# Kernel optimization log

Measured on AMD Instinct MI355X. Metric: run time of the kernel, lower is better.

The kernel has to match this reference:

```python
import jax, jax.numpy as jnp
import numpy as np

B, T, C = 4, 2048, 1024
N_HEAD = 16
HEAD = C // N_HEAD  # 64


def _rope_tables(T, dim, base=10000.0):
    inv_freq = 1.0 / (base ** (jnp.arange(0, dim, 2, dtype=jnp.float32) / dim))
    t = jnp.arange(T, dtype=jnp.float32)
    freqs = jnp.einsum('i,j->ij', t, inv_freq)           # [T, dim/2]
    emb = jnp.concatenate([freqs, freqs], axis=-1)        # [T, dim]
    return jnp.cos(emb), jnp.sin(emb)                     # each [T, dim]


def _rotate_half(x):
    x1, x2 = x[..., : x.shape[-1] // 2], x[..., x.shape[-1] // 2:]
    return jnp.concatenate([-x2, x1], axis=-1)


def setup_inputs() -> dict:
    key = jax.random.key(0)
    ks = jax.random.split(key, 4)
    x = jax.random.normal(ks[0], (B, T, C), dtype=jnp.float32)
    w_attn = jax.random.normal(ks[1], (C, 3 * C), dtype=jnp.float32) * (1.0 / np.sqrt(C))
    b_attn = jnp.zeros((3 * C,), dtype=jnp.float32)
    w_proj = jax.random.normal(ks[2], (C, C), dtype=jnp.float32) * (1.0 / np.sqrt(C))
    b_proj = jnp.zeros((C,), dtype=jnp.float32)
    return {"x": x, "w_attn": w_attn, "b_attn": b_attn, "w_proj": w_proj, "b_proj": b_proj}


def reference(x, w_attn, b_attn, w_proj, b_proj):
    Bx, Tx, Cx = x.shape
    qkv = x @ w_attn + b_attn                             # [B,T,3C]
    q, k, v = jnp.split(qkv, 3, axis=-1)
    # [B,T,C] -> [B,H,T,hd]
    def to_heads(t):
        return t.reshape(Bx, Tx, N_HEAD, HEAD).transpose(0, 2, 1, 3)
    q, k, v = to_heads(q), to_heads(k), to_heads(v)
    cos, sin = _rope_tables(Tx, HEAD)                     # [T,hd]
    cos = cos[None, None, :, :]
    sin = sin[None, None, :, :]
    q = q * cos + _rotate_half(q) * sin
    k = k * cos + _rotate_half(k) * sin
    scale = 1.0 / np.sqrt(HEAD)
    att = jnp.einsum('bhqd,bhkd->bhqk', q, k) * scale     # [B,H,T,T]
    causal = jnp.tril(jnp.ones((Tx, Tx), dtype=bool))
    att = jnp.where(causal[None, None], att, -jnp.inf)
    att = jax.nn.softmax(att, axis=-1)
    y = jnp.einsum('bhqk,bhkd->bhqd', att, v)             # [B,H,T,hd]
    y = y.transpose(0, 2, 1, 3).reshape(Bx, Tx, Cx)
    return y @ w_proj + b_proj
```

## Files before the change

### kernel.cpp

```cpp
#include <hip/hip_runtime.h>

#define B_  4
#define T_  2048
#define C_  1024
#define NH_ 16
#define HD_ 64
#define BT_ (B_*T_)
#define N3C (3*C_)

typedef _Float16 f16;
typedef _Float16 half8 __attribute__((ext_vector_type(8)));
typedef _Float16 half4 __attribute__((ext_vector_type(4)));
typedef float f32x4 __attribute__((ext_vector_type(4)));

__device__ __forceinline__ void gld16(const f16* g, f16* l) {
  __builtin_amdgcn_global_load_lds(
      (const __attribute__((address_space(1))) unsigned int*)g,
      (__attribute__((address_space(3))) unsigned int*)l, 16, 0, 0);
}

__global__ __launch_bounds__(256) void cvt_x(const float* __restrict__ X,
                                             f16* __restrict__ X16)
{
  const int i = blockIdx.x * 256 + threadIdx.x;
  const float4 a = ((const float4*)X)[i * 2];
  const float4 b = ((const float4*)X)[i * 2 + 1];
  half8 h;
  h[0] = (f16)a.x; h[1] = (f16)a.y; h[2] = (f16)a.z; h[3] = (f16)a.w;
  h[4] = (f16)b.x; h[5] = (f16)b.y; h[6] = (f16)b.z; h[7] = (f16)b.w;
  ((half8*)X16)[i] = h;
}

__global__ __launch_bounds__(256) void cvt_transpose(
    const float* __restrict__ W, f16* __restrict__ Wt, int K, int N)
{
  __shared__ float Ls[64][65];
  const int tid = threadIdx.x;
  const int n0 = blockIdx.x * 64, k0 = blockIdx.y * 64;
#pragma unroll
  for (int j = 0; j < 4; ++j) {
    const int idx = j * 256 + tid;
    const int r = idx >> 4, c = (idx & 15) * 4;
    const float4 w = *(const float4*)(W + (size_t)(k0 + r) * N + n0 + c);
    Ls[r][c + 0] = w.x; Ls[r][c + 1] = w.y; Ls[r][c + 2] = w.z; Ls[r][c + 3] = w.w;
  }
  __syncthreads();
#pragma unroll
  for (int j = 0; j < 2; ++j) {
    const int idx = j * 256 + tid;
    const int r = idx >> 3, c = (idx & 7) * 8;
    half8 h;
#pragma unroll
    for (int u = 0; u < 8; ++u) h[u] = (f16)Ls[c + u][r];
    *(half8*)(Wt + (size_t)(n0 + r) * K + k0 + c) = h;
  }
}

__global__ __launch_bounds__(256) void rope_tab(float2* __restrict__ cs)
{
  const int i = blockIdx.x * 256 + threadIdx.x;
  const int f = i & 31, t = i >> 5;
  const float inv = expf(-(2.0f * (float)f / 64.0f) * 9.210340371976184f);
  float sn, cn;
  sincosf((float)t * inv, &sn, &cn);
  cs[i] = make_float2(cn, sn);
}

__global__ __launch_bounds__(256) void gemm_qkv(
    const f16* __restrict__ A, const f16* __restrict__ Bt,
    const float* __restrict__ bias, const float2* __restrict__ cs,
    f16* __restrict__ Qo, f16* __restrict__ Ko, f16* __restrict__ Vt_g)
{
  __shared__ f16 As[128 * 64];
  __shared__ f16 Bs[128 * 64];
  const int tid  = threadIdx.x;
  const int row0 = blockIdx.y * 128;
  const int col0 = blockIdx.x * 128;
  const int wave = tid >> 6, lane = tid & 63;
  const int l = lane & 15, quad = lane >> 4;
  const int wm = wave >> 1, wn = wave & 1;
  const int sr = tid >> 3;
  const int scs = ((tid & 7) ^ (sr & 7)) * 8;
  const int lq7 = l & 7;

  f32x4 acc[4][4];
#pragma unroll
  for (int mi = 0; mi < 4; ++mi)
#pragma unroll
    for (int ni = 0; ni < 4; ++ni) acc[mi][ni] = (f32x4)0.0f;

  for (int k0 = 0; k0 < C_; k0 += 64) {
    __syncthreads();
#pragma unroll
    for (int p = 0; p < 4; ++p) {
      const int r = p * 32 + sr;
      gld16(A  + (size_t)(row0 + r) * C_ + k0 + scs, &As[p * 2048 + tid * 8]);
      gld16(Bt + (size_t)(col0 + r) * C_ + k0 + scs, &Bs[p * 2048 + tid * 8]);
    }
    __syncthreads();

#pragma unroll
    for (int s = 0; s < 2; ++s) {
      half8 af[4], bf[4];
#pragma unroll
      for (int mi = 0; mi < 4; ++mi)
        af[mi] = *(const half8*)&As[(wm * 64 + mi * 16 + l) * 64 + ((((s << 2) | quad) ^ lq7) << 3)];
#pragma unroll
      for (int ni = 0; ni < 4; ++ni)
        bf[ni] = *(const half8*)&Bs[(wn * 64 + ni * 16 + l) * 64 + ((((s << 2) | quad) ^ lq7) << 3)];
#pragma unroll
      for (int mi = 0; mi < 4; ++mi)
#pragma unroll
        for (int ni = 0; ni < 4; ++ni)
          acc[mi][ni] = __builtin_amdgcn_mfma_f32_16x16x32_f16(af[mi], bf[ni], acc[mi][ni], 0, 0, 0);
    }
  }

  const int region = col0 >> 10;
  const int colw = col0 + wn * 64;
  const int h = (colw & 1023) >> 6;
  if (region < 2) {
    f16* dst = (region == 0) ? Qo : Ko;
#pragma unroll
    for (int mi = 0; mi < 4; ++mi) {
#pragma unroll
      for (int r = 0; r < 4; ++r) {
        const int gm = row0 + wm * 64 + mi * 16 + quad * 4 + r;
        const int b = gm >> 11, t = gm & (T_ - 1);
        const size_t base = ((size_t)(b * NH_ + h) * T_ + t) * HD_;
        const float2* csrow = cs + t * 32;
#pragma unroll
        for (int ni = 0; ni < 2; ++ni) {
          const int d = ni * 16 + l;
          const float2 c2 = csrow[d];
          const float x1 = acc[mi][ni][r]     + bias[colw + d];
          const float x2 = acc[mi][ni + 2][r] + bias[colw + d + 32];
          dst[base + d]      = (f16)(x1 * c2.x - x2 * c2.y);
          dst[base + d + 32] = (f16)(x2 * c2.x + x1 * c2.y);
        }
      }
    }
  } else {
#pragma unroll
    for (int mi = 0; mi < 4; ++mi) {
      const int t0 = row0 + wm * 64 + mi * 16 + quad * 4;
      const int b = t0 >> 11, t = t0 & (T_ - 1);
#pragma unroll
      for (int ni = 0; ni < 4; ++ni) {
        const int d = ni * 16 + l;
        const float bs = bias[colw + d];
        half4 o;
#pragma unroll
        for (int r = 0; r < 4; ++r) o[r] = (f16)(acc[mi][ni][r] + bs);
        *(half4*)(Vt_g + ((size_t)((b * NH_ + h) * HD_ + d)) * T_ + t) = o;
      }
    }
  }
}

__global__ __launch_bounds__(256) void attn_mfma(
    const f16* __restrict__ Qg, const f16* __restrict__ Kg,
    const f16* __restrict__ Vt_g, f16* __restrict__ Y)
{
  __shared__ f16 Ks[64 * 64];
  __shared__ f16 Vt[64 * 64];
  const int tid  = threadIdx.x;
  const int qt   = 15 - (blockIdx.x >> 6);
  const int bh   = blockIdx.x & 63;
  const int b    = bh >> 4, h = bh & 15;
  const int wave = tid >> 6, lane = tid & 63;
  const int l    = lane & 15, quad = lane >> 4;
  const int lq7  = l & 7;
  int qrow[2];
  qrow[0] = qt * 128 + wave * 16 + l;
  qrow[1] = qrow[0] + 64;

  half8 qf[2][2];
#pragma unroll
  for (int u = 0; u < 2; ++u) {
    const f16* qp = Qg + ((size_t)bh * T_ + qrow[u]) * HD_;
#pragma unroll
    for (int s = 0; s < 2; ++s)
      qf[u][s] = *(const half8*)(qp + s * 32 + quad * 8);
  }

  f32x4 O[2][4];
#pragma unroll
  for (int u = 0; u < 2; ++u)
#pragma unroll
    for (int mi = 0; mi < 4; ++mi) O[u][mi] = (f32x4)0.0f;
  float l_run[2] = {0.f, 0.f};

  const float c1 = 0.125f * 1.44269504f;
  const float c2 = -4.0f  * 1.44269504f;

  const f16* kbase  = Kg   + (size_t)bh * T_ * HD_;
  const f16* vtbase = Vt_g + (size_t)bh * HD_ * T_;

  const int nkt = 2 * qt + 2;
  for (int kt = 0; kt < nkt; ++kt) {
    __syncthreads();
#pragma unroll
    for (int i = 0; i < 2; ++i) {
      const int r = i * 32 + (tid >> 3);
      const int c = tid & 7;
      const int cst = ((c ^ (r & 7)) << 3);
      const half8 hk = *(const half8*)(kbase + (size_t)(kt * 64 + r) * HD_ + c * 8);
      *(half8*)&Ks[r * 64 + cst] = hk;
      const half8 hv = *(const half8*)(vtbase + (size_t)r * T_ + kt * 64 + c * 8);
      *(half8*)&Vt[r * 64 + cst] = hv;
    }
    __syncthreads();

    f32x4 St[2][4];
#pragma unroll
    for (int u = 0; u < 2; ++u)
#pragma unroll
      for (int st = 0; st < 4; ++st) St[u][st] = (f32x4)0.0f;
#pragma unroll
    for (int st = 0; st < 4; ++st) {
#pragma unroll
      for (int s = 0; s < 2; ++s) {
        const int row = st * 16 + l;
        const half8 af = *(const half8*)&Ks[row * 64 + ((((s << 2) | quad) ^ lq7) << 3)];
#pragma unroll
        for (int u = 0; u < 2; ++u)
          St[u][st] = __builtin_amdgcn_mfma_f32_16x16x32_f16(af, qf[u][s], St[u][st], 0, 0, 0);
      }
    }

    const bool domask = (kt >= 2 * qt);
    const int k0 = kt * 64;
    half4 pf[2][4];
#pragma unroll
    for (int u = 0; u < 2; ++u) {
      float psum = 0.f;
#pragma unroll
      for (int st = 0; st < 4; ++st) {
        float pv[4];
#pragma unroll
        for (int r = 0; r < 4; ++r) {
          float x = fmaf(St[u][st][r], c1, c2);
          if (domask) {
            const int key = k0 + st * 16 + quad * 4 + r;
            if (key > qrow[u]) x = -1e9f;
          }
          const float ev = exp2f(x);
          pv[r] = ev;
          psum += ev;
        }
        pf[u][st][0] = (f16)pv[0]; pf[u][st][1] = (f16)pv[1];
        pf[u][st][2] = (f16)pv[2]; pf[u][st][3] = (f16)pv[3];
      }
      l_run[u] += psum;
    }

#pragma unroll
    for (int mi = 0; mi < 4; ++mi) {
      const int row = mi * 16 + l;
#pragma unroll
      for (int ki = 0; ki < 4; ++ki) {
        const int kch = (ki << 1) | (quad >> 1);
        const half4 vf = *(const half4*)&Vt[row * 64 + ((kch ^ lq7) << 3) + ((quad & 1) << 2)];
#pragma unroll
        for (int u = 0; u < 2; ++u)
          O[u][mi] = __builtin_amdgcn_mfma_f32_16x16x16f16(vf, pf[u][ki], O[u][mi], 0, 0, 0);
      }
    }
  }

#pragma unroll
  for (int u = 0; u < 2; ++u) {
    float lt = l_run[u];
    lt += __shfl_xor(lt, 16);
    lt += __shfl_xor(lt, 32);
    const float inv = 1.0f / lt;
    f16* yp = Y + ((size_t)(b * T_) + qrow[u]) * C_ + h * 64;
#pragma unroll
    for (int mi = 0; mi < 4; ++mi) {
      half4 o;
      o[0] = (f16)(O[u][mi][0] * inv); o[1] = (f16)(O[u][mi][1] * inv);
      o[2] = (f16)(O[u][mi][2] * inv); o[3] = (f16)(O[u][mi][3] * inv);
      *(half4*)(yp + mi * 16 + quad * 4) = o;
    }
  }
}

__global__ __launch_bounds__(256) void gemm_proj(
    const f16* __restrict__ A, const f16* __restrict__ Bt,
    const float* __restrict__ bias, float* __restrict__ Out)
{
  __shared__ f16 As[128 * 64];
  __shared__ f16 Bs[128 * 64];
  const int tid  = threadIdx.x;
  const int row0 = blockIdx.y * 128;
  const int col0 = blockIdx.x * 128;
  const int wave = tid >> 6, lane = tid & 63;
  const int l = lane & 15, quad = lane >> 4;
  const int wm = wave >> 1, wn = wave & 1;
  const int sr = tid >> 3;
  const int scs = ((tid & 7) ^ (sr & 7)) * 8;
  const int lq7 = l & 7;

  f32x4 acc[4][4];
#pragma unroll
  for (int mi = 0; mi < 4; ++mi)
#pragma unroll
    for (int ni = 0; ni < 4; ++ni) acc[mi][ni] = (f32x4)0.0f;

  for (int k0 = 0; k0 < C_; k0 += 64) {
    __syncthreads();
#pragma unroll
    for (int p = 0; p < 4; ++p) {
      const int r = p * 32 + sr;
      gld16(A  + (size_t)(row0 + r) * C_ + k0 + scs, &As[p * 2048 + tid * 8]);
      gld16(Bt + (size_t)(col0 + r) * C_ + k0 + scs, &Bs[p * 2048 + tid * 8]);
    }
    __syncthreads();

#pragma unroll
    for (int s = 0; s < 2; ++s) {
      half8 af[4], bf[4];
#pragma unroll
      for (int mi = 0; mi < 4; ++mi)
        af[mi] = *(const half8*)&As[(wm * 64 + mi * 16 + l) * 64 + ((((s << 2) | quad) ^ lq7) << 3)];
#pragma unroll
      for (int ni = 0; ni < 4; ++ni)
        bf[ni] = *(const half8*)&Bs[(wn * 64 + ni * 16 + l) * 64 + ((((s << 2) | quad) ^ lq7) << 3)];
#pragma unroll
      for (int mi = 0; mi < 4; ++mi)
#pragma unroll
        for (int ni = 0; ni < 4; ++ni)
          acc[mi][ni] = __builtin_amdgcn_mfma_f32_16x16x32_f16(af[mi], bf[ni], acc[mi][ni], 0, 0, 0);
    }
  }

#pragma unroll
  for (int mi = 0; mi < 4; ++mi) {
#pragma unroll
    for (int ni = 0; ni < 4; ++ni) {
#pragma unroll
      for (int r = 0; r < 4; ++r) {
        const int gm = row0 + wm * 64 + mi * 16 + quad * 4 + r;
        const int n  = col0 + wn * 64 + ni * 16 + l;
        Out[(size_t)gm * C_ + n] = acc[mi][ni][r] + bias[n];
      }
    }
  }
}

extern "C" void kernel_launch(void* const* d_in, const int* in_sizes, int n_in,
                              void* d_out, int out_size, void* d_ws, size_t ws_size,
                              hipStream_t stream) {
  const float* x      = (const float*)d_in[0];
  const float* w_attn = (const float*)d_in[1];
  const float* b_attn = (const float*)d_in[2];
  const float* w_proj = (const float*)d_in[3];
  const float* b_proj = (const float*)d_in[4];
  float* out = (float*)d_out;

  const size_t elems = (size_t)BT_ * C_;
  f16* x16 = (f16*)d_ws;
  f16* wta = x16 + elems;
  f16* wtp = wta + (size_t)N3C * C_;
  f16* q   = wtp + (size_t)C_ * C_;
  f16* k   = q + elems;
  f16* vt  = k + elems;
  f16* y   = vt + elems;
  float2* cs = (float2*)(y + elems);

  rope_tab<<<dim3((T_ * 32) / 256), 256, 0, stream>>>(cs);
  cvt_x<<<dim3(elems / 8 / 256), 256, 0, stream>>>(x, x16);
  cvt_transpose<<<dim3(N3C / 64, C_ / 64), 256, 0, stream>>>(w_attn, wta, C_, N3C);
  cvt_transpose<<<dim3(C_ / 64, C_ / 64), 256, 0, stream>>>(w_proj, wtp, C_, C_);
  gemm_qkv<<<dim3(N3C / 128, BT_ / 128), 256, 0, stream>>>(x16, wta, b_attn, cs, q, k, vt);
  attn_mfma<<<dim3(16 * 64), 256, 0, stream>>>(q, k, vt, y);
  gemm_proj<<<dim3(C_ / 128, BT_ / 128), 256, 0, stream>>>(y, wtp, b_proj, out);
}
```

Measured before the change: 294.2 us.

## Double-buffer attention K/V tiles, fold softmax scale into Q, merge prep kernels

```diff
diff --git a/kernel.cpp b/kernel.cpp
--- a/kernel.cpp
+++ b/kernel.cpp
@@ -19,24 +19,39 @@
       (__attribute__((address_space(3))) unsigned int*)l, 16, 0, 0);
 }
 
-__global__ __launch_bounds__(256) void cvt_x(const float* __restrict__ X,
-                                             f16* __restrict__ X16)
-{
-  const int i = blockIdx.x * 256 + threadIdx.x;
-  const float4 a = ((const float4*)X)[i * 2];
-  const float4 b = ((const float4*)X)[i * 2 + 1];
-  half8 h;
-  h[0] = (f16)a.x; h[1] = (f16)a.y; h[2] = (f16)a.z; h[3] = (f16)a.w;
-  h[4] = (f16)b.x; h[5] = (f16)b.y; h[6] = (f16)b.z; h[7] = (f16)b.w;
-  ((half8*)X16)[i] = h;
-}
-
-__global__ __launch_bounds__(256) void cvt_transpose(
-    const float* __restrict__ W, f16* __restrict__ Wt, int K, int N)
+__global__ __launch_bounds__(256) void prep(
+    const float* __restrict__ X, f16* __restrict__ X16,
+    const float* __restrict__ Wa, f16* __restrict__ Wta,
+    const float* __restrict__ Wp, f16* __restrict__ Wtp,
+    float2* __restrict__ cs)
 {
   __shared__ float Ls[64][65];
   const int tid = threadIdx.x;
-  const int n0 = blockIdx.x * 64, k0 = blockIdx.y * 64;
+  const int blk = blockIdx.x;
+  if (blk < 4096) {
+    const int i = blk * 256 + tid;
+    const float4 a = ((const float4*)X)[i * 2];
+    const float4 b = ((const float4*)X)[i * 2 + 1];
+    half8 hx;
+    hx[0] = (f16)a.x; hx[1] = (f16)a.y; hx[2] = (f16)a.z; hx[3] = (f16)a.w;
+    hx[4] = (f16)b.x; hx[5] = (f16)b.y; hx[6] = (f16)b.z; hx[7] = (f16)b.w;
+    ((half8*)X16)[i] = hx;
+    return;
+  }
+  if (blk >= 5120) {
+    const int i = (blk - 5120) * 256 + tid;
+    const int f = i & 31, t = i >> 5;
+    const float inv = expf(-(2.0f * (float)f / 64.0f) * 9.210340371976184f);
+    float sn, cn;
+    sincosf((float)t * inv, &sn, &cn);
+    cs[i] = make_float2(cn, sn);
+    return;
+  }
+  const float* W; f16* Wt; int N, i2;
+  if (blk < 4864) { W = Wa; Wt = Wta; N = N3C; i2 = blk - 4096; }
+  else            { W = Wp; Wt = Wtp; N = C_;  i2 = blk - 4864; }
+  const int nblk = N >> 6;
+  const int n0 = (i2 % nblk) * 64, k0 = (i2 / nblk) * 64;
 #pragma unroll
   for (int j = 0; j < 4; ++j) {
     const int idx = j * 256 + tid;
@@ -49,21 +64,11 @@
   for (int j = 0; j < 2; ++j) {
     const int idx = j * 256 + tid;
     const int r = idx >> 3, c = (idx & 7) * 8;
-    half8 h;
-#pragma unroll
-    for (int u = 0; u < 8; ++u) h[u] = (f16)Ls[c + u][r];
-    *(half8*)(Wt + (size_t)(n0 + r) * K + k0 + c) = h;
-  }
-}
-
-__global__ __launch_bounds__(256) void rope_tab(float2* __restrict__ cs)
-{
-  const int i = blockIdx.x * 256 + threadIdx.x;
-  const int f = i & 31, t = i >> 5;
-  const float inv = expf(-(2.0f * (float)f / 64.0f) * 9.210340371976184f);
-  float sn, cn;
-  sincosf((float)t * inv, &sn, &cn);
-  cs[i] = make_float2(cn, sn);
+    half8 hw;
+#pragma unroll
+    for (int u = 0; u < 8; ++u) hw[u] = (f16)Ls[c + u][r];
+    *(half8*)(Wt + (size_t)(n0 + r) * C_ + k0 + c) = hw;
+  }
 }
 
 __global__ __launch_bounds__(256) void gemm_qkv(
@@ -121,6 +126,7 @@
   const int h = (colw & 1023) >> 6;
   if (region < 2) {
     f16* dst = (region == 0) ? Qo : Ko;
+    const float qs = (region == 0) ? 0.18033688f : 1.0f;
 #pragma unroll
     for (int mi = 0; mi < 4; ++mi) {
 #pragma unroll
@@ -135,8 +141,8 @@
           const float2 c2 = csrow[d];
           const float x1 = acc[mi][ni][r]     + bias[colw + d];
           const float x2 = acc[mi][ni + 2][r] + bias[colw + d + 32];
-          dst[base + d]      = (f16)(x1 * c2.x - x2 * c2.y);
-          dst[base + d + 32] = (f16)(x2 * c2.x + x1 * c2.y);
+          dst[base + d]      = (f16)((x1 * c2.x - x2 * c2.y) * qs);
+          dst[base + d + 32] = (f16)((x2 * c2.x + x1 * c2.y) * qs);
         }
       }
     }
@@ -162,8 +168,8 @@
     const f16* __restrict__ Qg, const f16* __restrict__ Kg,
     const f16* __restrict__ Vt_g, f16* __restrict__ Y)
 {
-  __shared__ f16 Ks[64 * 64];
-  __shared__ f16 Vt[64 * 64];
+  __shared__ f16 Ks[2][64 * 64];
+  __shared__ f16 Vt[2][64 * 64];
   const int tid  = threadIdx.x;
   const int qt   = 15 - (blockIdx.x >> 6);
   const int bh   = blockIdx.x & 63;
@@ -191,26 +197,38 @@
     for (int mi = 0; mi < 4; ++mi) O[u][mi] = (f32x4)0.0f;
   float l_run[2] = {0.f, 0.f};
 
-  const float c1 = 0.125f * 1.44269504f;
-  const float c2 = -4.0f  * 1.44269504f;
-
   const f16* kbase  = Kg   + (size_t)bh * T_ * HD_;
   const f16* vtbase = Vt_g + (size_t)bh * HD_ * T_;
+  const int r0 = tid >> 3, cc = tid & 7;
 
   const int nkt = 2 * qt + 2;
+  half8 hk[2], hv[2];
+#pragma unroll
+  for (int i = 0; i < 2; ++i) {
+    const int r = i * 32 + r0;
+    hk[i] = *(const half8*)(kbase + (size_t)r * HD_ + cc * 8);
+    hv[i] = *(const half8*)(vtbase + (size_t)r * T_ + cc * 8);
+  }
+
   for (int kt = 0; kt < nkt; ++kt) {
-    __syncthreads();
+    f16* KsB = Ks[kt & 1];
+    f16* VtB = Vt[kt & 1];
 #pragma unroll
     for (int i = 0; i < 2; ++i) {
-      const int r = i * 32 + (tid >> 3);
-      const int c = tid & 7;
-      const int cst = ((c ^ (r & 7)) << 3);
-      const half8 hk = *(const half8*)(kbase + (size_t)(kt * 64 + r) * HD_ + c * 8);
-      *(half8*)&Ks[r * 64 + cst] = hk;
-      const half8 hv = *(const half8*)(vtbase + (size_t)r * T_ + kt * 64 + c * 8);
-      *(half8*)&Vt[r * 64 + cst] = hv;
-    }
-    __syncthreads();
+      const int r = i * 32 + r0;
+      const int cst = ((cc ^ (r & 7)) << 3);
+      *(half8*)&KsB[r * 64 + cst] = hk[i];
+      *(half8*)&VtB[r * 64 + cst] = hv[i];
+    }
+    __syncthreads();
+    if (kt + 1 < nkt) {
+#pragma unroll
+      for (int i = 0; i < 2; ++i) {
+        const int r = i * 32 + r0;
+        hk[i] = *(const half8*)(kbase + (size_t)((kt + 1) * 64 + r) * HD_ + cc * 8);
+        hv[i] = *(const half8*)(vtbase + (size_t)r * T_ + (kt + 1) * 64 + cc * 8);
+      }
+    }
 
     f32x4 St[2][4];
 #pragma unroll
@@ -222,7 +240,7 @@
 #pragma unroll
       for (int s = 0; s < 2; ++s) {
         const int row = st * 16 + l;
-        const half8 af = *(const half8*)&Ks[row * 64 + ((((s << 2) | quad) ^ lq7) << 3)];
+        const half8 af = *(const half8*)&KsB[row * 64 + ((((s << 2) | quad) ^ lq7) << 3)];
 #pragma unroll
         for (int u = 0; u < 2; ++u)
           St[u][st] = __builtin_amdgcn_mfma_f32_16x16x32_f16(af, qf[u][s], St[u][st], 0, 0, 0);
@@ -240,7 +258,7 @@
         float pv[4];
 #pragma unroll
         for (int r = 0; r < 4; ++r) {
-          float x = fmaf(St[u][st][r], c1, c2);
+          float x = St[u][st][r];
           if (domask) {
             const int key = k0 + st * 16 + quad * 4 + r;
             if (key > qrow[u]) x = -1e9f;
@@ -261,7 +279,7 @@
 #pragma unroll
       for (int ki = 0; ki < 4; ++ki) {
         const int kch = (ki << 1) | (quad >> 1);
-        const half4 vf = *(const half4*)&Vt[row * 64 + ((kch ^ lq7) << 3) + ((quad & 1) << 2)];
+        const half4 vf = *(const half4*)&VtB[row * 64 + ((kch ^ lq7) << 3) + ((quad & 1) << 2)];
 #pragma unroll
         for (int u = 0; u < 2; ++u)
           O[u][mi] = __builtin_amdgcn_mfma_f32_16x16x16f16(vf, pf[u][ki], O[u][mi], 0, 0, 0);
@@ -369,10 +387,7 @@
   f16* y   = vt + elems;
   float2* cs = (float2*)(y + elems);
 
-  rope_tab<<<dim3((T_ * 32) / 256), 256, 0, stream>>>(cs);
-  cvt_x<<<dim3(elems / 8 / 256), 256, 0, stream>>>(x, x16);
-  cvt_transpose<<<dim3(N3C / 64, C_ / 64), 256, 0, stream>>>(w_attn, wta, C_, N3C);
-  cvt_transpose<<<dim3(C_ / 64, C_ / 64), 256, 0, stream>>>(w_proj, wtp, C_, C_);
+  prep<<<dim3(5376), 256, 0, stream>>>(x, x16, w_attn, wta, w_proj, wtp, cs);
   gemm_qkv<<<dim3(N3C / 128, BT_ / 128), 256, 0, stream>>>(x16, wta, b_attn, cs, q, k, vt);
   attn_mfma<<<dim3(16 * 64), 256, 0, stream>>>(q, k, vt, y);
   gemm_proj<<<dim3(C_ / 128, BT_ / 128), 256, 0, stream>>>(y, wtp, b_proj, out);
```

Measured after the change: 271.4 us. 1.08x faster.
